# Performance work log

Hardware: AMD Instinct MI355X
Metric: run time of the kernel (lower is better)

## Reference

```python
import jax, jax.numpy as jnp
import numpy as np

D_MODEL, H, D_FF = 1024, 16, 4096
D_K = D_MODEL // H
EPS = 1e-6
NEG = -1e9


def _layer_norm(x, alpha, bias):
    # torch LayerNormalization: scalar alpha/bias, unbiased std (ddof=1), eps added to std
    n = x.shape[-1]
    mu = jnp.mean(x, axis=-1, keepdims=True)
    var = jnp.sum((x - mu) ** 2, axis=-1, keepdims=True) / (n - 1)
    std = jnp.sqrt(var)
    return alpha * (x - mu) / (std + EPS) + bias


def _linear(x, w, b):
    # torch nn.Linear: y = x @ W^T + b, W: [out, in]
    return jnp.einsum('bsd,od->bso', x, w) + b


def setup_inputs() -> dict:
    key = jax.random.key(0)
    ks = jax.random.split(key, 12)
    d, dff = D_MODEL, D_FF
    s_d = 1.0 / np.sqrt(d)
    s_ff = 1.0 / np.sqrt(dff)
    inp = {
        'x': jax.random.normal(ks[0], (2, 2048, d), dtype=jnp.float32),
        'mask': jnp.ones((2, 1, 1, 2048), dtype=jnp.int32),
        'wq': jax.random.uniform(ks[1], (d, d), jnp.float32, -s_d, s_d),
        'bq': jnp.zeros((d,), jnp.float32),
        'wk': jax.random.uniform(ks[2], (d, d), jnp.float32, -s_d, s_d),
        'bk': jnp.zeros((d,), jnp.float32),
        'wv': jax.random.uniform(ks[3], (d, d), jnp.float32, -s_d, s_d),
        'bv': jnp.zeros((d,), jnp.float32),
        'wo': jax.random.uniform(ks[4], (d, d), jnp.float32, -s_d, s_d),
        'bo': jnp.zeros((d,), jnp.float32),
        'w1': jax.random.uniform(ks[5], (dff, d), jnp.float32, -s_d, s_d),
        'b1': jnp.zeros((dff,), jnp.float32),
        'w2': jax.random.uniform(ks[6], (d, dff), jnp.float32, -s_ff, s_ff),
        'b2': jnp.zeros((d,), jnp.float32),
        'ln1_a': jnp.ones((1,), jnp.float32),
        'ln1_b': jnp.zeros((1,), jnp.float32),
        'ln2_a': jnp.ones((1,), jnp.float32),
        'ln2_b': jnp.zeros((1,), jnp.float32),
    }
    return inp


def reference(x, mask, wq, bq, wk, bk, wv, bv, wo, bo, w1, b1, w2, b2,
              ln1_a, ln1_b, ln2_a, ln2_b):
    b, s, d = x.shape

    # --- residual 1: pre-norm self-attention (dropout is identity in eval) ---
    xn = _layer_norm(x, ln1_a, ln1_b)
    q = _linear(xn, wq, bq).reshape(b, s, H, D_K).transpose(0, 2, 1, 3)  # [b,h,s,dk]
    k = _linear(xn, wk, bk).reshape(b, s, H, D_K).transpose(0, 2, 1, 3)
    v = _linear(xn, wv, bv).reshape(b, s, H, D_K).transpose(0, 2, 1, 3)
    scores = jnp.einsum('bhqd,bhkd->bhqk', q, k) / jnp.sqrt(jnp.float32(D_K))
    scores = jnp.where(mask == 0, NEG, scores)
    p = jax.nn.softmax(scores, axis=-1)
    attn = jnp.einsum('bhqk,bhkd->bhqd', p, v)
    attn = attn.transpose(0, 2, 1, 3).reshape(b, s, d)
    x = x + _linear(attn, wo, bo)

    # --- residual 2: pre-norm feed-forward ---
    xn = _layer_norm(x, ln2_a, ln2_b)
    h = jax.nn.relu(_linear(xn, w1, b1))
    x = x + _linear(h, w2, b2)
    return x
```

## Files before the change

kernel.cpp:

```cpp
#include <hip/hip_runtime.h>
#include <hip/hip_bf16.h>
#include <stdint.h>

typedef __bf16 bf16x8 __attribute__((ext_vector_type(8)));
typedef __bf16 bf16x4 __attribute__((ext_vector_type(4)));
typedef short  s16x4  __attribute__((ext_vector_type(4)));
typedef float  f32x4  __attribute__((ext_vector_type(4)));
typedef unsigned short u16;

__device__ __forceinline__ u16 f2bf(float f) {
    return __builtin_bit_cast(u16, (__bf16)f);
}

__device__ __forceinline__ f32x4 vmax4(f32x4 a, f32x4 b) {
    f32x4 r;
    r[0] = fmaxf(a[0], b[0]); r[1] = fmaxf(a[1], b[1]);
    r[2] = fmaxf(a[2], b[2]); r[3] = fmaxf(a[3], b[3]);
    return r;
}
__device__ __forceinline__ f32x4 vexp4(f32x4 a) {
    f32x4 r;
    r[0] = __expf(a[0]); r[1] = __expf(a[1]);
    r[2] = __expf(a[2]); r[3] = __expf(a[3]);
    return r;
}

__device__ __forceinline__ f32x4 mfma16(bf16x4 a, bf16x4 b, f32x4 c) {
#if __has_builtin(__builtin_amdgcn_mfma_f32_16x16x16bf16_1k)
    return __builtin_amdgcn_mfma_f32_16x16x16bf16_1k(
        __builtin_bit_cast(s16x4, a), __builtin_bit_cast(s16x4, b), c, 0, 0, 0);
#else
    f32x4 d;
    asm volatile("v_mfma_f32_16x16x16_bf16 %0, %1, %2, %3"
                 : "=v"(d) : "v"(a), "v"(b), "v"(c));
    return d;
#endif
}

__device__ __forceinline__ void stage16(const void* g, void* lds_wave_base) {
#if __has_builtin(__builtin_amdgcn_global_load_lds)
    __builtin_amdgcn_global_load_lds(
        (const __attribute__((address_space(1))) void*)g,
        (__attribute__((address_space(3))) void*)lds_wave_base, 16, 0, 0);
#else
    int lane = threadIdx.x & 63;
    *(uint4*)((char*)lds_wave_base + lane * 16) = *(const uint4*)g;
#endif
}

__device__ __forceinline__ int swz(int r) {
    return (((r) & 7) ^ (((r) >> 3) & 7)) << 4;
}

__global__ void pack1_kernel(const float* __restrict__ wq, const float* __restrict__ wk,
                             const float* __restrict__ wv, const float* __restrict__ bq,
                             const float* __restrict__ bk, const float* __restrict__ bv,
                             const float* __restrict__ wo,
                             u16* __restrict__ wqkv, float* __restrict__ bqkv,
                             u16* __restrict__ wo_b) {
    const float QS = 0.125f;
    size_t i0 = (size_t)blockIdx.x * 256 + threadIdx.x;
    size_t stride = (size_t)gridDim.x * 256;
    const size_t DD = 1024u * 1024u;
    for (size_t i = i0; i < 3 * DD; i += stride) {
        float v;
        if (i < DD)          v = wq[i] * QS;
        else if (i < 2 * DD) v = wk[i - DD];
        else                 v = wv[i - 2 * DD];
        wqkv[i] = f2bf(v);
    }
    for (size_t i = i0; i < DD; i += stride) wo_b[i] = f2bf(wo[i]);
    for (size_t i = i0; i < 3072; i += stride)
        bqkv[i] = (i < 1024) ? bq[i] * QS : ((i < 2048) ? bk[i - 1024] : bv[i - 2048]);
}

__global__ void pack2_kernel(const float* __restrict__ w1, const float* __restrict__ w2,
                             u16* __restrict__ w1_b, u16* __restrict__ w2_b) {
    size_t i0 = (size_t)blockIdx.x * 256 + threadIdx.x;
    size_t stride = (size_t)gridDim.x * 256;
    const size_t DD = 1024u * 1024u;
    for (size_t i = i0; i < 4 * DD; i += stride) w1_b[i] = f2bf(w1[i]);
    for (size_t i = i0; i < 4 * DD; i += stride) w2_b[i] = f2bf(w2[i]);
}

__global__ __launch_bounds__(256)
void ln_kernel(const float* __restrict__ x, u16* __restrict__ out,
               const float* __restrict__ alpha, const float* __restrict__ beta) {
    const int row = blockIdx.x;
    const int t = threadIdx.x, lane = t & 63, w = t >> 6;
    float4 v = ((const float4*)(x + (size_t)row * 1024))[t];
    float s  = v.x + v.y + v.z + v.w;
    float ss = v.x * v.x + v.y * v.y + v.z * v.z + v.w * v.w;
#pragma unroll
    for (int d = 1; d < 64; d <<= 1) { s += __shfl_xor(s, d); ss += __shfl_xor(ss, d); }
    __shared__ float red[8];
    if (lane == 0) { red[w] = s; red[4 + w] = ss; }
    __syncthreads();
    s  = red[0] + red[1] + red[2] + red[3];
    ss = red[4] + red[5] + red[6] + red[7];
    const float mu  = s * (1.f / 1024.f);
    const float var = fmaxf((ss - 1024.f * mu * mu) * (1.f / 1023.f), 0.f);
    const float inv = alpha[0] / (sqrtf(var) + 1e-6f);
    const float bb  = beta[0];
    ushort4 o;
    o.x = f2bf((v.x - mu) * inv + bb);
    o.y = f2bf((v.y - mu) * inv + bb);
    o.z = f2bf((v.z - mu) * inv + bb);
    o.w = f2bf((v.w - mu) * inv + bb);
    ((ushort4*)(out + (size_t)row * 1024))[t] = o;
}

template <int EPI>
__global__ __launch_bounds__(256)
void gemm_bt(const u16* __restrict__ A, const u16* __restrict__ B,
             const float* __restrict__ bias, const float* __restrict__ resid,
             void* __restrict__ Cout, int M, int N, int K, int ldc) {
    __shared__ __align__(16) char As[16384];
    __shared__ __align__(16) char Bs[16384];
    const int t = threadIdx.x;
    const int lane = t & 63, wave = t >> 6;
    const int g = lane >> 4, c = lane & 15;
    const int wm = wave >> 1, wn = wave & 1;
    const int bm = blockIdx.x, bn = blockIdx.y;

    const f32x4 z4 = {0.f, 0.f, 0.f, 0.f};
    f32x4 acc[4][4];
#pragma unroll
    for (int m = 0; m < 4; ++m)
#pragma unroll
        for (int n = 0; n < 4; ++n) acc[m][n] = z4;

    const int srow = t >> 2;
    const int ak = (((t & 3) ^ ((t >> 2) & 3)) << 3);
    const u16* ga = A + (size_t)(bm * 128 + srow) * K + ak;
    const u16* gb = B + (size_t)(bn * 128 + srow) * K + ak;
    const size_t rstep = (size_t)64 * K;

    auto STAGE = [&](int k0, int buf) {
        char* la = As + buf * 8192 + wave * 1024;
        char* lb = Bs + buf * 8192 + wave * 1024;
        stage16(ga + k0,         la);
        stage16(ga + k0 + rstep, la + 4096);
        stage16(gb + k0,         lb);
        stage16(gb + k0 + rstep, lb + 4096);
    };

    STAGE(0, 0);
    asm volatile("s_waitcnt vmcnt(0)" ::: "memory");
    __syncthreads();

    int cur = 0;
    for (int k0 = 0; k0 < K; k0 += 32) {
        if (k0 + 32 < K) STAGE(k0 + 32, cur ^ 1);
        const char* Ac = As + cur * 8192;
        const char* Bc = Bs + cur * 8192;
        bf16x8 a[4], b[4];
#pragma unroll
        for (int m = 0; m < 4; ++m) {
            int r = wm * 64 + m * 16 + c;
            a[m] = *(const bf16x8*)(Ac + r * 64 + ((g * 16) ^ ((c & 3) << 4)));
        }
#pragma unroll
        for (int n = 0; n < 4; ++n) {
            int r = wn * 64 + n * 16 + c;
            b[n] = *(const bf16x8*)(Bc + r * 64 + ((g * 16) ^ ((c & 3) << 4)));
        }
        __builtin_amdgcn_s_setprio(1);
#pragma unroll
        for (int m = 0; m < 4; ++m)
#pragma unroll
            for (int n = 0; n < 4; ++n)
                acc[m][n] = __builtin_amdgcn_mfma_f32_16x16x32_bf16(a[m], b[n], acc[m][n], 0, 0, 0);
        __builtin_amdgcn_s_setprio(0);
        asm volatile("s_waitcnt vmcnt(0)" ::: "memory");
        __syncthreads();
        cur ^= 1;
    }

    const int row0 = bm * 128 + wm * 64;
    const int col0 = bn * 128 + wn * 64;
#pragma unroll
    for (int m = 0; m < 4; ++m) {
#pragma unroll
        for (int n = 0; n < 4; ++n) {
            const int cc = col0 + n * 16 + c;
            const float bv = bias[cc];
#pragma unroll
            for (int j = 0; j < 4; ++j) {
                const int rr = row0 + m * 16 + g * 4 + j;
                float v = acc[m][n][j] + bv;
                if (EPI == 1) v = v > 0.f ? v : 0.f;
                if (EPI == 2) {
                    ((float*)Cout)[(size_t)rr * ldc + cc] = resid[(size_t)rr * ldc + cc] + v;
                } else {
                    ((u16*)Cout)[(size_t)rr * ldc + cc] = f2bf(v);
                }
            }
        }
    }
}

__global__ __launch_bounds__(256)
void attn_kernel(const u16* __restrict__ qkv, const int* __restrict__ mask,
                 u16* __restrict__ attn_out) {
    __shared__ __align__(16) char Ksm[32768];
    __shared__ __align__(16) char Vsm[16384];
    const int t = threadIdx.x, lane = t & 63, w = t >> 6;
    const int g = lane >> 4, c = lane & 15;
    const int flat = blockIdx.x;
    const int xcd = flat & 7, u = flat >> 3;
    const int qt = u & 31;
    const int p = xcd * 4 + (u >> 5);
    const int h = p & 15, b = p >> 4;
    const int S = 2048, LD = 3072;
    const int NT = S / 128;

    bf16x8 qf[2];
#pragma unroll
    for (int half = 0; half < 2; ++half)
        qf[half] = *(const bf16x8*)&qkv[(size_t)(b * S + qt * 64 + w * 16 + c) * LD
                                        + h * 64 + half * 32 + g * 8];

    const f32x4 z4 = {0.f, 0.f, 0.f, 0.f};
    f32x4 accO[4];
#pragma unroll
    for (int dt = 0; dt < 4; ++dt) accO[dt] = z4;
    float mrun = -1e30f, lrun = 0.f;

    unsigned vr[2][8];
    const int vd0 = (t & 31) * 2;
    const int vkg[2] = {t >> 5, 8 + (t >> 5)};

    auto STAGEK = [&](int kt, char* Kd) {
#pragma unroll
        for (int it = 0; it < 4; ++it) {
            int idx = it * 256 + t;
            int k = idx >> 3, pp = idx & 7;
            int ps = pp ^ ((k & 7) ^ ((k >> 3) & 7));
            stage16(&qkv[(size_t)(b * S + kt * 128 + k) * LD + 1024 + h * 64 + ps * 8],
                    Kd + (it * 256 + w * 64) * 16);
        }
    };
    auto VLOAD = [&](int kt) {
#pragma unroll
        for (int it = 0; it < 2; ++it) {
            const u16* src = &qkv[(size_t)(b * S + kt * 128 + vkg[it] * 8) * LD + 2048 + h * 64 + vd0];
#pragma unroll
            for (int i = 0; i < 8; ++i)
                vr[it][i] = *(const unsigned*)(src + (size_t)i * LD);
        }
    };
    auto VWRITE = [&]() {
#pragma unroll
        for (int it = 0; it < 2; ++it) {
            int d0 = vd0, kg = vkg[it];
            uint4 lo, hi;
            lo.x = (vr[it][0] & 0xffffu) | (vr[it][1] << 16);
            lo.y = (vr[it][2] & 0xffffu) | (vr[it][3] << 16);
            lo.z = (vr[it][4] & 0xffffu) | (vr[it][5] << 16);
            lo.w = (vr[it][6] & 0xffffu) | (vr[it][7] << 16);
            hi.x = (vr[it][0] >> 16) | (vr[it][1] & 0xffff0000u);
            hi.y = (vr[it][2] >> 16) | (vr[it][3] & 0xffff0000u);
            hi.z = (vr[it][4] >> 16) | (vr[it][5] & 0xffff0000u);
            hi.w = (vr[it][6] >> 16) | (vr[it][7] & 0xffff0000u);
            *(uint4*)(Vsm + d0 * 256 + ((kg * 16) ^ swz(d0)))           = lo;
            *(uint4*)(Vsm + (d0 + 1) * 256 + ((kg * 16) ^ swz(d0 + 1))) = hi;
        }
    };

    STAGEK(0, Ksm);
    VLOAD(0);
    asm volatile("s_waitcnt vmcnt(0)" ::: "memory");
    VWRITE();
    __syncthreads();

    int cur = 0;
    for (int kt = 0; kt < NT; ++kt) {
        char* Kc = Ksm + cur * 16384;
        if (kt + 1 < NT) {
            STAGEK(kt + 1, Ksm + (cur ^ 1) * 16384);
            VLOAD(kt + 1);
        }

        f32x4 s[8];
        __builtin_amdgcn_s_setprio(1);
#pragma unroll
        for (int n = 0; n < 8; ++n) {
            int kr = n * 16 + c;
            bf16x8 k0 = *(const bf16x8*)(Kc + kr * 128 + ((g * 16) ^ swz(kr)));
            bf16x8 k1 = *(const bf16x8*)(Kc + kr * 128 + ((64 + g * 16) ^ swz(kr)));
            s[n] = __builtin_amdgcn_mfma_f32_16x16x32_bf16(k0, qf[0], z4, 0, 0, 0);
            s[n] = __builtin_amdgcn_mfma_f32_16x16x32_bf16(k1, qf[1], s[n], 0, 0, 0);
        }
        __builtin_amdgcn_s_setprio(0);
#pragma unroll
        for (int n = 0; n < 8; ++n) {
            int4 mv = *(const int4*)&mask[b * S + kt * 128 + n * 16 + g * 4];
            if (mv.x == 0) s[n][0] = -1e9f;
            if (mv.y == 0) s[n][1] = -1e9f;
            if (mv.z == 0) s[n][2] = -1e9f;
            if (mv.w == 0) s[n][3] = -1e9f;
        }
        {
            f32x4 pm4 = s[0];
#pragma unroll
            for (int n = 1; n < 8; ++n) pm4 = vmax4(pm4, s[n]);
            float pm = fmaxf(fmaxf(pm4[0], pm4[1]), fmaxf(pm4[2], pm4[3]));
            pm = fmaxf(pm, __shfl_xor(pm, 16));
            pm = fmaxf(pm, __shfl_xor(pm, 32));
            float mn = fmaxf(mrun, pm);
            float sc = __expf(mrun - mn);
            mrun = mn;
            f32x4 mn4 = {mn, mn, mn, mn};
            f32x4 ps4 = z4;
#pragma unroll
            for (int n = 0; n < 8; ++n) { s[n] = vexp4(s[n] - mn4); ps4 += s[n]; }
            float ps = ps4[0] + ps4[1] + ps4[2] + ps4[3];
            ps += __shfl_xor(ps, 16);
            ps += __shfl_xor(ps, 32);
            lrun = lrun * sc + ps;
#pragma unroll
            for (int dt = 0; dt < 4; ++dt) accO[dt] *= sc;
        }
        __builtin_amdgcn_s_setprio(1);
#pragma unroll
        for (int n = 0; n < 8; ++n) {
            bf16x4 p0;
#pragma unroll
            for (int j = 0; j < 4; ++j) p0[j] = (__bf16)s[n][j];
#pragma unroll
            for (int dt = 0; dt < 4; ++dt) {
                int d = dt * 16 + c;
                bf16x4 vf = *(const bf16x4*)(Vsm + d * 256 + ((n * 32 + g * 8) ^ swz(d)));
                accO[dt] = mfma16(vf, p0, accO[dt]);
            }
        }
        __builtin_amdgcn_s_setprio(0);

        __syncthreads();
        asm volatile("s_waitcnt vmcnt(0)" ::: "memory");
        if (kt + 1 < NT) VWRITE();
        __syncthreads();
        cur ^= 1;
    }

    char* Osm = Ksm;
    {
        float inv = 1.f / lrun;
        int ql = w * 16 + c;
#pragma unroll
        for (int dt = 0; dt < 4; ++dt)
#pragma unroll
            for (int j = 0; j < 4; ++j) {
                int d = dt * 16 + g * 4 + j;
                *(u16*)(Osm + ql * 128 + ((d * 2) ^ swz(ql))) = f2bf(accO[dt][j] * inv);
            }
    }
    __syncthreads();
#pragma unroll
    for (int it = 0; it < 2; ++it) {
        int idx = it * 256 + t;
        int q = idx >> 3, pp = idx & 7;
        uint4 val = *(const uint4*)(Osm + q * 128 + ((pp * 16) ^ swz(q)));
        *(uint4*)&attn_out[(size_t)(b * S + qt * 64 + q) * 1024 + h * 64 + pp * 8] = val;
    }
}

extern "C" void kernel_launch(void* const* d_in, const int* in_sizes, int n_in,
                              void* d_out, int out_size, void* d_ws, size_t ws_size,
                              hipStream_t stream) {
    const float* x    = (const float*)d_in[0];
    const int*   mask = (const int*)d_in[1];
    const float* wq   = (const float*)d_in[2];
    const float* bq   = (const float*)d_in[3];
    const float* wk   = (const float*)d_in[4];
    const float* bk   = (const float*)d_in[5];
    const float* wv   = (const float*)d_in[6];
    const float* bv   = (const float*)d_in[7];
    const float* wo   = (const float*)d_in[8];
    const float* bo   = (const float*)d_in[9];
    const float* w1   = (const float*)d_in[10];
    const float* b1   = (const float*)d_in[11];
    const float* w2   = (const float*)d_in[12];
    const float* b2   = (const float*)d_in[13];
    const float* ln1a = (const float*)d_in[14];
    const float* ln1b = (const float*)d_in[15];
    const float* ln2a = (const float*)d_in[16];
    const float* ln2b = (const float*)d_in[17];

    const size_t MB = 1048576;
    char* ws = (char*)d_ws;
    const bool big = ws_size >= 88 * MB;

    u16 *xn, *wqkv, *wo_b, *qkvb, *attnb, *w1_b, *w2_b, *hbuf;
    float *bqkv, *x1;
    int nchunk;
    if (big) {
        xn    = (u16*)(ws + 0 * MB);
        wqkv  = (u16*)(ws + 8 * MB);
        wo_b  = (u16*)(ws + 14 * MB);
        qkvb  = (u16*)(ws + 16 * MB);
        attnb = (u16*)(ws + 40 * MB);
        x1    = (float*)(ws + 48 * MB);
        w1_b  = (u16*)(ws + 64 * MB);
        w2_b  = (u16*)(ws + 72 * MB);
        hbuf  = (u16*)(ws + 16 * MB);
        bqkv  = (float*)(ws + 80 * MB);
        nchunk = 1;
    } else {
        xn    = (u16*)(ws + 0 * MB);
        wqkv  = (u16*)(ws + 8 * MB);
        wo_b  = (u16*)(ws + 14 * MB);
        qkvb  = (u16*)(ws + 16 * MB);
        attnb = (u16*)(ws + 40 * MB);
        x1    = (float*)(ws + 16 * MB);
        w1_b  = (u16*)(ws + 32 * MB);
        w2_b  = (u16*)(ws + 8 * MB);
        hbuf  = (u16*)(ws + 40 * MB);
        bqkv  = (float*)(ws + 40 * MB);
        nchunk = 4;
    }

    pack1_kernel<<<1024, 256, 0, stream>>>(wq, wk, wv, bq, bk, bv, wo, wqkv, bqkv, wo_b);
    ln_kernel<<<4096, 256, 0, stream>>>(x, xn, ln1a, ln1b);
    gemm_bt<0><<<dim3(32, 24), 256, 0, stream>>>(xn, wqkv, bqkv, nullptr, qkvb,
                                                 4096, 3072, 1024, 3072);
    attn_kernel<<<1024, 256, 0, stream>>>(qkvb, mask, attnb);
    gemm_bt<2><<<dim3(32, 8), 256, 0, stream>>>(attnb, wo_b, bo, x, x1,
                                                4096, 1024, 1024, 1024);
    pack2_kernel<<<1024, 256, 0, stream>>>(w1, w2, w1_b, w2_b);
    ln_kernel<<<4096, 256, 0, stream>>>(x1, xn, ln2a, ln2b);

    const int mrows = 4096 / nchunk;
    for (int cidx = 0; cidx < nchunk; ++cidx) {
        const size_t ro = (size_t)cidx * mrows;
        gemm_bt<1><<<dim3(mrows / 128, 32), 256, 0, stream>>>(
            xn + ro * 1024, w1_b, b1, nullptr, hbuf, mrows, 4096, 1024, 4096);
        gemm_bt<2><<<dim3(mrows / 128, 8), 256, 0, stream>>>(
            hbuf, w2_b, b2, x1 + ro * 1024, (float*)d_out + ro * 1024,
            mrows, 1024, 4096, 1024);
    }
}
```

Baseline: 309.5 us.

## Add 256x256-tile 512-thread GEMM for QKV and FFN1 projections

Adds a new GEMM kernel using 256x256 output tiles per block with 8 waves, 128KB of dynamic LDS double-buffered with swizzled layout, phased A/B prefetch interleaved with MFMA work, and s_setprio around the MFMA bursts. It is used for the QKV projection and, when the workspace is large, the FFN up-projection, replacing the 128x128 tile kernel. The larger tiles raise arithmetic intensity and cut global traffic per FLOP. In exchange the grid is small (192/256 blocks, one block per CU given LDS use), which risks poor latency hiding and wave-quantization tails.

```diff
diff --git a/kernel.cpp b/kernel.cpp
--- a/kernel.cpp
+++ b/kernel.cpp
@@ -195,6 +195,110 @@
                 } else {
                     ((u16*)Cout)[(size_t)rr * ldc + cc] = f2bf(v);
                 }
+            }
+        }
+    }
+}
+
+template <int EPI>
+__global__ __launch_bounds__(512)
+void gemm256(const u16* __restrict__ A, const u16* __restrict__ B,
+             const float* __restrict__ bias, u16* __restrict__ Cout,
+             int K, int ldc, int gm) {
+    extern __shared__ __align__(16) char lds[];
+    char* As0 = lds;
+    char* Bs0 = lds + 65536;
+    const int t = threadIdx.x, lane = t & 63, wave = t >> 6;
+    const int g = lane >> 4, c = lane & 15;
+    const int wm = wave >> 2, wn = wave & 3;
+    const int f = blockIdx.x, nb = gridDim.x;
+    const int sw = (f & 7) * (nb >> 3) + (f >> 3);
+    const int bm = sw % gm, bn = sw / gm;
+
+    const f32x4 z4 = {0.f, 0.f, 0.f, 0.f};
+    f32x4 acc[8][4];
+#pragma unroll
+    for (int mi = 0; mi < 8; ++mi)
+#pragma unroll
+        for (int ni = 0; ni < 4; ++ni) acc[mi][ni] = z4;
+
+    auto STAGE = [&](const u16* G, int base_row, int k0, char* dst, int half) {
+#pragma unroll
+        for (int l = 0; l < 2; ++l) {
+            int idx = half * 1024 + l * 512 + t;
+            int row = idx >> 3, p = idx & 7;
+            stage16(G + (size_t)(base_row + row) * K + k0 + ((p ^ (row & 7)) << 3),
+                    dst + (half * 1024 + l * 512 + wave * 64) * 16);
+        }
+    };
+    auto ldA = [&](int buf, int mi, int ks) -> bf16x8 {
+        int r = wm * 128 + mi * 16 + c;
+        return *(const bf16x8*)(As0 + buf * 32768 + r * 128 + ((((ks << 2) + g) ^ (r & 7)) << 4));
+    };
+    auto ldB = [&](int buf, int ni, int ks) -> bf16x8 {
+        int r = wn * 64 + ni * 16 + c;
+        return *(const bf16x8*)(Bs0 + buf * 32768 + r * 128 + ((((ks << 2) + g) ^ (r & 7)) << 4));
+    };
+
+    const int NT = K >> 6;
+    STAGE(A, bm * 256, 0, As0, 0); STAGE(A, bm * 256, 0, As0, 1);
+    STAGE(B, bn * 256, 0, Bs0, 0); STAGE(B, bn * 256, 0, Bs0, 1);
+    asm volatile("s_waitcnt vmcnt(0)" ::: "memory");
+    __builtin_amdgcn_s_barrier();
+
+    int cur = 0;
+    for (int kt = 0; kt < NT; ++kt) {
+        const int k0n = (kt + 1) << 6;
+        const bool more = kt + 1 < NT;
+        bf16x8 bfr[4][2];
+#pragma unroll
+        for (int ni = 0; ni < 4; ++ni) {
+            bfr[ni][0] = ldB(cur, ni, 0);
+            bfr[ni][1] = ldB(cur, ni, 1);
+        }
+#pragma unroll
+        for (int ph = 0; ph < 4; ++ph) {
+            bf16x8 a0k0 = ldA(cur, 2 * ph, 0),     a0k1 = ldA(cur, 2 * ph, 1);
+            bf16x8 a1k0 = ldA(cur, 2 * ph + 1, 0), a1k1 = ldA(cur, 2 * ph + 1, 1);
+            if (more && ph == 0) {
+                STAGE(A, bm * 256, k0n, As0 + (cur ^ 1) * 32768, 0);
+                STAGE(A, bm * 256, k0n, As0 + (cur ^ 1) * 32768, 1);
+            }
+            if (more && ph == 1) {
+                STAGE(B, bn * 256, k0n, Bs0 + (cur ^ 1) * 32768, 0);
+                STAGE(B, bn * 256, k0n, Bs0 + (cur ^ 1) * 32768, 1);
+            }
+            __builtin_amdgcn_s_barrier();
+            __builtin_amdgcn_s_setprio(1);
+#pragma unroll
+            for (int ni = 0; ni < 4; ++ni) {
+                acc[2 * ph][ni]     = __builtin_amdgcn_mfma_f32_16x16x32_bf16(a0k0, bfr[ni][0], acc[2 * ph][ni], 0, 0, 0);
+                acc[2 * ph][ni]     = __builtin_amdgcn_mfma_f32_16x16x32_bf16(a0k1, bfr[ni][1], acc[2 * ph][ni], 0, 0, 0);
+                acc[2 * ph + 1][ni] = __builtin_amdgcn_mfma_f32_16x16x32_bf16(a1k0, bfr[ni][0], acc[2 * ph + 1][ni], 0, 0, 0);
+                acc[2 * ph + 1][ni] = __builtin_amdgcn_mfma_f32_16x16x32_bf16(a1k1, bfr[ni][1], acc[2 * ph + 1][ni], 0, 0, 0);
+            }
+            __builtin_amdgcn_s_setprio(0);
+            __builtin_amdgcn_s_barrier();
+        }
+        asm volatile("s_waitcnt vmcnt(0)" ::: "memory");
+        __builtin_amdgcn_s_barrier();
+        cur ^= 1;
+    }
+
+    const int row0 = bm * 256 + wm * 128;
+    const int col0 = bn * 256 + wn * 64;
+#pragma unroll
+    for (int mi = 0; mi < 8; ++mi) {
+#pragma unroll
+        for (int ni = 0; ni < 4; ++ni) {
+            const int cc = col0 + ni * 16 + c;
+            const float bv = bias[cc];
+#pragma unroll
+            for (int j = 0; j < 4; ++j) {
+                const int rr = row0 + mi * 16 + g * 4 + j;
+                float v = acc[mi][ni][j] + bv;
+                if (EPI == 1) v = v > 0.f ? v : 0.f;
+                Cout[(size_t)rr * ldc + cc] = f2bf(v);
             }
         }
     }
@@ -391,6 +495,11 @@
     const size_t MB = 1048576;
     char* ws = (char*)d_ws;
     const bool big = ws_size >= 88 * MB;
+
+    hipFuncSetAttribute(reinterpret_cast<const void*>(gemm256<0>),
+                        hipFuncAttributeMaxDynamicSharedMemorySize, 131072);
+    hipFuncSetAttribute(reinterpret_cast<const void*>(gemm256<1>),
+                        hipFuncAttributeMaxDynamicSharedMemorySize, 131072);
 
     u16 *xn, *wqkv, *wo_b, *qkvb, *attnb, *w1_b, *w2_b, *hbuf;
     float *bqkv, *x1;
@@ -423,21 +532,26 @@
 
     pack1_kernel<<<1024, 256, 0, stream>>>(wq, wk, wv, bq, bk, bv, wo, wqkv, bqkv, wo_b);
     ln_kernel<<<4096, 256, 0, stream>>>(x, xn, ln1a, ln1b);
-    gemm_bt<0><<<dim3(32, 24), 256, 0, stream>>>(xn, wqkv, bqkv, nullptr, qkvb,
-                                                 4096, 3072, 1024, 3072);
+    gemm256<0><<<192, 512, 131072, stream>>>(xn, wqkv, bqkv, qkvb, 1024, 3072, 16);
     attn_kernel<<<1024, 256, 0, stream>>>(qkvb, mask, attnb);
     gemm_bt<2><<<dim3(32, 8), 256, 0, stream>>>(attnb, wo_b, bo, x, x1,
                                                 4096, 1024, 1024, 1024);
     pack2_kernel<<<1024, 256, 0, stream>>>(w1, w2, w1_b, w2_b);
     ln_kernel<<<4096, 256, 0, stream>>>(x1, xn, ln2a, ln2b);
 
-    const int mrows = 4096 / nchunk;
-    for (int cidx = 0; cidx < nchunk; ++cidx) {
-        const size_t ro = (size_t)cidx * mrows;
-        gemm_bt<1><<<dim3(mrows / 128, 32), 256, 0, stream>>>(
-            xn + ro * 1024, w1_b, b1, nullptr, hbuf, mrows, 4096, 1024, 4096);
-        gemm_bt<2><<<dim3(mrows / 128, 8), 256, 0, stream>>>(
-            hbuf, w2_b, b2, x1 + ro * 1024, (float*)d_out + ro * 1024,
-            mrows, 1024, 4096, 1024);
-    }
-}
+    if (big) {
+        gemm256<1><<<256, 512, 131072, stream>>>(xn, w1_b, b1, hbuf, 1024, 4096, 16);
+        gemm_bt<2><<<dim3(32, 8), 256, 0, stream>>>(hbuf, w2_b, b2, x1, (float*)d_out,
+                                                    4096, 1024, 4096, 1024);
+    } else {
+        const int mrows = 4096 / nchunk;
+        for (int cidx = 0; cidx < nchunk; ++cidx) {
+            const size_t ro = (size_t)cidx * mrows;
+            gemm_bt<1><<<dim3(mrows / 128, 32), 256, 0, stream>>>(
+                xn + ro * 1024, w1_b, b1, nullptr, hbuf, mrows, 4096, 1024, 4096);
+            gemm_bt<2><<<dim3(mrows / 128, 8), 256, 0, stream>>>(
+                hbuf, w2_b, b2, x1 + ro * 1024, (float*)d_out + ro * 1024,
+                mrows, 1024, 4096, 1024);
+        }
+    }
+}
```

New measurement: 298.1 us. 1.04x faster.
